# Kernel optimization log

Measured on AMD Instinct MI355X. Metric: run time of the kernel, lower is better.

Reference implementation:

```python
import jax, jax.numpy as jnp
import numpy as np

T, B, N, D = 32, 8, 256, 512
TAU = 2.0   # LIF membrane time constant
VTH = 1.0   # spike threshold
ALPHA = 4.0 # surrogate-gradient sharpness


def setup_inputs() -> dict:
    key = jax.random.key(0)
    k0, k1, k2 = jax.random.split(key, 3)
    scale = 1.0 / np.sqrt(D)
    return {
        "x": jax.random.normal(k0, (T, B, N, D), jnp.float32),
        "tr_mx": jnp.zeros((B, N, D), jnp.float32),            # initial membrane state
        "W_lif": jax.random.normal(k1, (D, D), jnp.float32) * scale,
        "b_lif": jnp.zeros((D,), jnp.float32),
        "W_rec": jax.random.normal(k2, (D, D), jnp.float32) * scale,  # recon2 weight (d_ff=D -> patch_size=D)
        "b_rec": jnp.zeros((D,), jnp.float32),
    }


def _spike(v):
    # Heaviside forward, sigmoid surrogate backward (standard SNN straight-through)
    s = jax.nn.sigmoid(ALPHA * v)
    return s + jax.lax.stop_gradient((v > 0).astype(v.dtype) - s)


def reference(x, tr_mx, W_lif, b_lif, W_rec, b_rec):
    # MemoryUpdate.replay: tau-decayed LIF recurrence over time, emitting spike gate per step
    inp = jnp.einsum('tbnd,de->tbne', x, W_lif) + b_lif   # [T,B,N,D] input current

    def step(mem, i_t):
        mem = mem + (i_t - mem) / TAU        # leaky integration
        sp = _spike(mem - VTH)               # fire
        mem = mem * (1.0 - sp)               # hard reset
        return mem, sp

    _, sp_seq = jax.lax.scan(step, tr_mx, inp)  # sp_seq: [T,B,N,D]

    g = x * (1.0 - sp_seq)                       # gated residual
    rec_x = jnp.einsum('tbnd,dp->tbnp', g, W_rec) + b_rec  # recon2 on flattened (T*B, N, D)
    return rec_x
```

## Files before the change

### kernel.cpp

```cpp
#include <hip/hip_runtime.h>
#include <hip/hip_bf16.h>


#define TT 32
#define CH 8
#define BB 8
#define NN 256
#define DD 512

typedef __attribute__((ext_vector_type(8))) short short8;
typedef __attribute__((ext_vector_type(4))) float f32x4;

__device__ __forceinline__ unsigned short f2bf(float f) {
    __hip_bfloat16 h = __float2bfloat16(f);
    return *reinterpret_cast<unsigned short*>(&h);
}

__global__ void cast_transpose_wr(const float* __restrict__ Wr,
                                  unsigned short* __restrict__ Wt) {
    int idx = blockIdx.x * 256 + threadIdx.x;
    int d = idx >> 9;
    int p = idx & 511;
    Wt[p * DD + d] = f2bf(Wr[idx]);
}

template<bool UW>
__global__ __launch_bounds__(128, 2) void lif_decoder_v7(
    const float* __restrict__ x,
    const float* __restrict__ tr_mx,
    const float* __restrict__ Wl,
    const float* __restrict__ bl,
    const float* __restrict__ Wr,
    const float* __restrict__ br,
    const unsigned short* __restrict__ Wt,
    float* __restrict__ out)
{
    __shared__ __align__(16) float xs[CH * DD];
    __shared__ __align__(16) unsigned msk[DD];

    const int tid = threadIdx.x;
    const int tok = blockIdx.x;
    const int e0  = tid * 4;
    const size_t base = (size_t)tok * DD;
    const size_t st   = (size_t)BB * NN * DD;

    {
        float acc[CH][4];
        float4 m4 = *reinterpret_cast<const float4*>(&tr_mx[base + e0]);
        float m[4] = {m4.x, m4.y, m4.z, m4.w};
        unsigned mc[4] = {0u, 0u, 0u, 0u};

        const float4 blv = *reinterpret_cast<const float4*>(&bl[e0]);
        const float blr[4] = {blv.x, blv.y, blv.z, blv.w};

        #pragma unroll 1
        for (int tg = 0; tg < 4; ++tg) {
            #pragma unroll
            for (int r = 0; r < 8; ++r) {
                const int flat = r * 128 + tid;
                const int tl = flat >> 7;
                const int c4 = flat & 127;
                const float4 v = *reinterpret_cast<const float4*>(
                    &x[(size_t)(tg * CH + tl) * st + base + c4 * 4]);
                *reinterpret_cast<float4*>(&xs[tl * DD + c4 * 4]) = v;
            }
            __syncthreads();

            #pragma unroll
            for (int i = 0; i < CH; ++i)
                #pragma unroll
                for (int e = 0; e < 4; ++e) acc[i][e] = blr[e];

            #pragma unroll 2
            for (int d = 0; d < DD; d += 4) {
                const float4 w0 = *reinterpret_cast<const float4*>(&Wl[(size_t)(d + 0) * DD + e0]);
                const float4 w1 = *reinterpret_cast<const float4*>(&Wl[(size_t)(d + 1) * DD + e0]);
                const float4 w2 = *reinterpret_cast<const float4*>(&Wl[(size_t)(d + 2) * DD + e0]);
                const float4 w3 = *reinterpret_cast<const float4*>(&Wl[(size_t)(d + 3) * DD + e0]);
                #pragma unroll
                for (int i = 0; i < CH; ++i) {
                    const float4 xv = *reinterpret_cast<const float4*>(&xs[i * DD + d]);
                    acc[i][0] = fmaf(xv.x, w0.x, acc[i][0]);
                    acc[i][1] = fmaf(xv.x, w0.y, acc[i][1]);
                    acc[i][2] = fmaf(xv.x, w0.z, acc[i][2]);
                    acc[i][3] = fmaf(xv.x, w0.w, acc[i][3]);
                    acc[i][0] = fmaf(xv.y, w1.x, acc[i][0]);
                    acc[i][1] = fmaf(xv.y, w1.y, acc[i][1]);
                    acc[i][2] = fmaf(xv.y, w1.z, acc[i][2]);
                    acc[i][3] = fmaf(xv.y, w1.w, acc[i][3]);
                    acc[i][0] = fmaf(xv.z, w2.x, acc[i][0]);
                    acc[i][1] = fmaf(xv.z, w2.y, acc[i][1]);
                    acc[i][2] = fmaf(xv.z, w2.z, acc[i][2]);
                    acc[i][3] = fmaf(xv.z, w2.w, acc[i][3]);
                    acc[i][0] = fmaf(xv.w, w3.x, acc[i][0]);
                    acc[i][1] = fmaf(xv.w, w3.y, acc[i][1]);
                    acc[i][2] = fmaf(xv.w, w3.z, acc[i][2]);
                    acc[i][3] = fmaf(xv.w, w3.w, acc[i][3]);
                }
            }
            __syncthreads();

            #pragma unroll
            for (int i = 0; i < CH; ++i) {
                const int t = tg * CH + i;
                #pragma unroll
                for (int e = 0; e < 4; ++e) {
                    m[e] = m[e] + (acc[i][e] - m[e]) * 0.5f;
                    const float s = (m[e] - 1.0f > 0.0f) ? 1.0f : 0.0f;
                    mc[e] |= (s > 0.0f) ? (1u << t) : 0u;
                    m[e] *= (1.0f - s);
                }
            }
        }

        #pragma unroll
        for (int e = 0; e < 4; ++e) msk[e0 + e] = mc[e];
    }
    __syncthreads();

    {
        const int lane = tid & 63;
        const int wv   = tid >> 6;
        const int lcol = lane & 15;
        const int lkg  = lane >> 4;
        const int tA   = wv * 16 + lcol;

        short8 af[16];
        #pragma unroll
        for (int ks = 0; ks < 16; ++ks) {
            const int kb = ks * 32 + lkg * 8;
            const float4 x0 = *reinterpret_cast<const float4*>(&x[(size_t)tA * st + base + kb]);
            const float4 x1 = *reinterpret_cast<const float4*>(&x[(size_t)tA * st + base + kb + 4]);
            const uint4 m0 = *reinterpret_cast<const uint4*>(&msk[kb]);
            const uint4 m1 = *reinterpret_cast<const uint4*>(&msk[kb + 4]);
            short8 a;
            a[0] = (short)f2bf(((m0.x >> tA) & 1u) ? 0.0f : x0.x);
            a[1] = (short)f2bf(((m0.y >> tA) & 1u) ? 0.0f : x0.y);
            a[2] = (short)f2bf(((m0.z >> tA) & 1u) ? 0.0f : x0.z);
            a[3] = (short)f2bf(((m0.w >> tA) & 1u) ? 0.0f : x0.w);
            a[4] = (short)f2bf(((m1.x >> tA) & 1u) ? 0.0f : x1.x);
            a[5] = (short)f2bf(((m1.y >> tA) & 1u) ? 0.0f : x1.y);
            a[6] = (short)f2bf(((m1.z >> tA) & 1u) ? 0.0f : x1.z);
            a[7] = (short)f2bf(((m1.w >> tA) & 1u) ? 0.0f : x1.w);
            af[ks] = a;
        }

        #pragma unroll 1
        for (int pass = 0; pass < 4; ++pass) {
            const int colb = pass * 128;
            f32x4 acc[8];
            #pragma unroll
            for (int nt = 0; nt < 8; ++nt) {
                const float b = br[colb + nt * 16 + lcol];
                acc[nt] = (f32x4){b, b, b, b};
            }

            #pragma unroll
            for (int ks = 0; ks < 16; ++ks) {
                const int kb = ks * 32 + lkg * 8;
                #pragma unroll
                for (int nt = 0; nt < 8; ++nt) {
                    const int col = colb + nt * 16 + lcol;
                    short8 bf;
                    if (UW) {
                        bf = *reinterpret_cast<const short8*>(&Wt[(size_t)col * DD + kb]);
                    } else {
                        #pragma unroll
                        for (int j = 0; j < 8; ++j)
                            bf[j] = (short)f2bf(Wr[(size_t)(kb + j) * DD + col]);
                    }
                    acc[nt] = __builtin_amdgcn_mfma_f32_16x16x32_bf16(af[ks], bf, acc[nt], 0, 0, 0);
                }
            }

            #pragma unroll
            for (int nt = 0; nt < 8; ++nt) {
                const int col = colb + nt * 16 + lcol;
                #pragma unroll
                for (int r = 0; r < 4; ++r) {
                    const int t = wv * 16 + lkg * 4 + r;
                    out[(size_t)t * st + base + col] = acc[nt][r];
                }
            }
        }
    }
}

extern "C" void kernel_launch(void* const* d_in, const int* in_sizes, int n_in,
                              void* d_out, int out_size, void* d_ws, size_t ws_size,
                              hipStream_t stream) {
    const float* x     = (const float*)d_in[0];
    const float* tr_mx = (const float*)d_in[1];
    const float* Wl    = (const float*)d_in[2];
    const float* bl    = (const float*)d_in[3];
    const float* Wr    = (const float*)d_in[4];
    const float* br    = (const float*)d_in[5];
    float* out = (float*)d_out;

    const size_t wt_bytes = (size_t)DD * DD * 2;
    dim3 grid(BB * NN);
    dim3 block(128);

    if (ws_size >= wt_bytes) {
        unsigned short* Wt = (unsigned short*)d_ws;
        cast_transpose_wr<<<dim3(1024), dim3(256), 0, stream>>>(Wr, Wt);
        lif_decoder_v7<true><<<grid, block, 0, stream>>>(x, tr_mx, Wl, bl, Wr, br, Wt, out);
    } else {
        lif_decoder_v7<false><<<grid, block, 0, stream>>>(x, tr_mx, Wl, bl, Wr, br, nullptr, out);
    }
}
```

Baseline: 768.4 us.

## Process two tokens per 256-thread block to share weight loads

```diff
diff --git a/kernel.cpp b/kernel.cpp
--- a/kernel.cpp
+++ b/kernel.cpp
@@ -25,7 +25,7 @@
 }
 
 template<bool UW>
-__global__ __launch_bounds__(128, 2) void lif_decoder_v7(
+__global__ __launch_bounds__(256, 4) void lif_decoder_v8(
     const float* __restrict__ x,
     const float* __restrict__ tr_mx,
     const float* __restrict__ Wl,
@@ -35,12 +35,14 @@
     const unsigned short* __restrict__ Wt,
     float* __restrict__ out)
 {
-    __shared__ __align__(16) float xs[CH * DD];
-    __shared__ __align__(16) unsigned msk[DD];
+    __shared__ __align__(16) float xs[2 * CH * DD];
+    __shared__ __align__(16) unsigned msk[2 * DD];
 
     const int tid = threadIdx.x;
-    const int tok = blockIdx.x;
-    const int e0  = tid * 4;
+    const int tg  = tid >> 7;
+    const int tl  = tid & 127;
+    const int e0  = tl * 4;
+    const int tok = blockIdx.x * 2 + tg;
     const size_t base = (size_t)tok * DD;
     const size_t st   = (size_t)BB * NN * DD;
 
@@ -54,15 +56,18 @@
         const float blr[4] = {blv.x, blv.y, blv.z, blv.w};
 
         #pragma unroll 1
-        for (int tg = 0; tg < 4; ++tg) {
+        for (int tgc = 0; tgc < 4; ++tgc) {
             #pragma unroll
             for (int r = 0; r < 8; ++r) {
-                const int flat = r * 128 + tid;
-                const int tl = flat >> 7;
-                const int c4 = flat & 127;
+                const int flat = r * 256 + tid;
+                const int q    = flat >> 10;
+                const int rem  = flat & 1023;
+                const int trow = rem >> 7;
+                const int c4   = rem & 127;
                 const float4 v = *reinterpret_cast<const float4*>(
-                    &x[(size_t)(tg * CH + tl) * st + base + c4 * 4]);
-                *reinterpret_cast<float4*>(&xs[tl * DD + c4 * 4]) = v;
+                    &x[(size_t)(tgc * CH + trow) * st
+                       + (size_t)(blockIdx.x * 2 + q) * DD + c4 * 4]);
+                *reinterpret_cast<float4*>(&xs[(q * CH + trow) * DD + c4 * 4]) = v;
             }
             __syncthreads();
 
@@ -70,6 +75,8 @@
             for (int i = 0; i < CH; ++i)
                 #pragma unroll
                 for (int e = 0; e < 4; ++e) acc[i][e] = blr[e];
+
+            const float* xsl = &xs[tg * CH * DD];
 
             #pragma unroll 2
             for (int d = 0; d < DD; d += 4) {
@@ -79,7 +86,7 @@
                 const float4 w3 = *reinterpret_cast<const float4*>(&Wl[(size_t)(d + 3) * DD + e0]);
                 #pragma unroll
                 for (int i = 0; i < CH; ++i) {
-                    const float4 xv = *reinterpret_cast<const float4*>(&xs[i * DD + d]);
+                    const float4 xv = *reinterpret_cast<const float4*>(&xsl[i * DD + d]);
                     acc[i][0] = fmaf(xv.x, w0.x, acc[i][0]);
                     acc[i][1] = fmaf(xv.x, w0.y, acc[i][1]);
                     acc[i][2] = fmaf(xv.x, w0.z, acc[i][2]);
@@ -102,7 +109,7 @@
 
             #pragma unroll
             for (int i = 0; i < CH; ++i) {
-                const int t = tg * CH + i;
+                const int t = tgc * CH + i;
                 #pragma unroll
                 for (int e = 0; e < 4; ++e) {
                     m[e] = m[e] + (acc[i][e] - m[e]) * 0.5f;
@@ -114,25 +121,29 @@
         }
 
         #pragma unroll
-        for (int e = 0; e < 4; ++e) msk[e0 + e] = mc[e];
+        for (int e = 0; e < 4; ++e) msk[tg * DD + e0 + e] = mc[e];
     }
     __syncthreads();
 
     {
+        const int wv   = tid >> 6;
         const int lane = tid & 63;
-        const int wv   = tid >> 6;
+        const int qB   = wv >> 1;
+        const int hB   = wv & 1;
         const int lcol = lane & 15;
         const int lkg  = lane >> 4;
-        const int tA   = wv * 16 + lcol;
+        const int tA   = hB * 16 + lcol;
+        const size_t baseB = (size_t)(blockIdx.x * 2 + qB) * DD;
+        const unsigned* mq = &msk[qB * DD];
 
         short8 af[16];
         #pragma unroll
         for (int ks = 0; ks < 16; ++ks) {
             const int kb = ks * 32 + lkg * 8;
-            const float4 x0 = *reinterpret_cast<const float4*>(&x[(size_t)tA * st + base + kb]);
-            const float4 x1 = *reinterpret_cast<const float4*>(&x[(size_t)tA * st + base + kb + 4]);
-            const uint4 m0 = *reinterpret_cast<const uint4*>(&msk[kb]);
-            const uint4 m1 = *reinterpret_cast<const uint4*>(&msk[kb + 4]);
+            const float4 x0 = *reinterpret_cast<const float4*>(&x[(size_t)tA * st + baseB + kb]);
+            const float4 x1 = *reinterpret_cast<const float4*>(&x[(size_t)tA * st + baseB + kb + 4]);
+            const uint4 m0 = *reinterpret_cast<const uint4*>(&mq[kb]);
+            const uint4 m1 = *reinterpret_cast<const uint4*>(&mq[kb + 4]);
             short8 a;
             a[0] = (short)f2bf(((m0.x >> tA) & 1u) ? 0.0f : x0.x);
             a[1] = (short)f2bf(((m0.y >> tA) & 1u) ? 0.0f : x0.y);
@@ -178,8 +189,8 @@
                 const int col = colb + nt * 16 + lcol;
                 #pragma unroll
                 for (int r = 0; r < 4; ++r) {
-                    const int t = wv * 16 + lkg * 4 + r;
-                    out[(size_t)t * st + base + col] = acc[nt][r];
+                    const int t = hB * 16 + lkg * 4 + r;
+                    out[(size_t)t * st + baseB + col] = acc[nt][r];
                 }
             }
         }
@@ -198,14 +209,14 @@
     float* out = (float*)d_out;
 
     const size_t wt_bytes = (size_t)DD * DD * 2;
-    dim3 grid(BB * NN);
-    dim3 block(128);
+    dim3 grid(BB * NN / 2);
+    dim3 block(256);
 
     if (ws_size >= wt_bytes) {
         unsigned short* Wt = (unsigned short*)d_ws;
         cast_transpose_wr<<<dim3(1024), dim3(256), 0, stream>>>(Wr, Wt);
-        lif_decoder_v7<true><<<grid, block, 0, stream>>>(x, tr_mx, Wl, bl, Wr, br, Wt, out);
+        lif_decoder_v8<true><<<grid, block, 0, stream>>>(x, tr_mx, Wl, bl, Wr, br, Wt, out);
     } else {
-        lif_decoder_v7<false><<<grid, block, 0, stream>>>(x, tr_mx, Wl, bl, Wr, br, nullptr, out);
+        lif_decoder_v8<false><<<grid, block, 0, stream>>>(x, tr_mx, Wl, bl, Wr, br, nullptr, out);
     }
 }
```

Result: slower. 976.7 us (+27.1%).
